# Optimization experiments

Measured on AMD Instinct MI355X. Metric: run time of the kernel, lower is better.

## Reference

```python
import jax, jax.numpy as jnp
import numpy as np


def setup_inputs() -> dict:
    key = jax.random.key(0)
    ks = jax.random.split(key, 8)
    B, E, L, D = 128, 512, 128, 128
    N = B * E
    return {
        "claim_vec": jax.random.normal(ks[0], (N, D), dtype=jnp.float32),
        "evidence_vec": jax.random.normal(ks[1], (N, D), dtype=jnp.float32),
        "ids_claim": jax.random.randint(ks[2], (N, L), 0, 30000, dtype=jnp.int64 if jax.config.jax_enable_x64 else jnp.int32),
        "ids_evidence": jax.random.randint(ks[3], (N, L), 0, 30000, dtype=jnp.int64 if jax.config.jax_enable_x64 else jnp.int32),
        "masks_claim": jax.random.randint(ks[4], (N, L), 0, 2, dtype=jnp.int64 if jax.config.jax_enable_x64 else jnp.int32),
        "masks_evidence": jax.random.randint(ks[5], (N, L), 0, 2, dtype=jnp.int64 if jax.config.jax_enable_x64 else jnp.int32),
        "token_claim": jax.random.randint(ks[6], (N, L), 0, 2, dtype=jnp.int64 if jax.config.jax_enable_x64 else jnp.int32),
        "token_evidence": jax.random.randint(ks[7], (N, L), 0, 2, dtype=jnp.int64 if jax.config.jax_enable_x64 else jnp.int32),
        "batchsize": 128,
        "evidences_num": 512,
        "top_k": 5,
        "max_len": 128,
    }


def reference(claim_vec, evidence_vec, ids_claim, ids_evidence,
              masks_claim, masks_evidence, token_claim, token_evidence,
              batchsize, evidences_num, top_k, max_len):
    B, E, K, L = batchsize, evidences_num, top_k, max_len
    eps = 1e-8
    # Cosine similarity per row (torch.F.cosine_similarity semantics: clamp each norm to eps)
    num = jnp.sum(claim_vec * evidence_vec, axis=-1)                      # [B*E]
    na = jnp.maximum(jnp.linalg.norm(claim_vec, axis=-1), eps)
    nb = jnp.maximum(jnp.linalg.norm(evidence_vec, axis=-1), eps)
    cos = (num / (na * nb)).reshape(B, E)
    cos_sim = jax.nn.softmax(cos, axis=1)
    top_cos, top_idx = jax.lax.top_k(cos_sim, K)                          # [B,K]

    def gather_ev(x):  # x: [B*E, L] -> top-k gathered, flattened [B*K, L]
        x3 = x.reshape(B, E, L)
        return jnp.take_along_axis(x3, top_idx[:, :, None], axis=1).reshape(-1, L)

    def slice_cl(x):   # claim side: first K rows per batch
        return x.reshape(B, E, L)[:, :K, :].reshape(-1, L)

    ids_retri = (slice_cl(ids_claim), gather_ev(ids_evidence))
    masks_retri = (slice_cl(masks_claim), gather_ev(masks_evidence))
    token_retri = (slice_cl(token_claim), gather_ev(token_evidence))
    return (top_cos, ids_retri[0], ids_retri[1], masks_retri[0], masks_retri[1],
            token_retri[0], token_retri[1])
```

## Files before the change

kernel.cpp:

```cpp
#include <hip/hip_runtime.h>
#include <hip/hip_bf16.h>
#include <math.h>

#define B_ 128
#define E_ 512
#define L_ 128
#define D_ 128
#define K_ 5
#define N_ (B_ * E_)
#define ROWOUT (B_ * K_)
#define OUT_TENSOR_SZ (ROWOUT * L_)

__global__ __launch_bounds__(256) void cos_kernel(const float* __restrict__ a,
                                                  const float* __restrict__ b,
                                                  float* __restrict__ cosout) {
    const int row  = blockIdx.x * 8 + (threadIdx.x >> 5);
    const int l32  = threadIdx.x & 31;
    const float4* a4 = reinterpret_cast<const float4*>(a) + (size_t)row * (D_ / 4) + l32;
    const float4* b4 = reinterpret_cast<const float4*>(b) + (size_t)row * (D_ / 4) + l32;
    float4 av = *a4;
    float4 bv = *b4;
    float dot = av.x * bv.x + av.y * bv.y + av.z * bv.z + av.w * bv.w;
    float na  = av.x * av.x + av.y * av.y + av.z * av.z + av.w * av.w;
    float nb  = bv.x * bv.x + bv.y * bv.y + bv.z * bv.z + bv.w * bv.w;
    #pragma unroll
    for (int o = 16; o; o >>= 1) {
        dot += __shfl_xor(dot, o);
        na  += __shfl_xor(na,  o);
        nb  += __shfl_xor(nb,  o);
    }
    if (l32 == 0) {
        const float eps = 1e-8f;
        float denom = fmaxf(sqrtf(na), eps) * fmaxf(sqrtf(nb), eps);
        cosout[row] = dot / denom;
    }
}

__global__ __launch_bounds__(512) void softmax_topk_gather_kernel(
        const float* __restrict__ cosv,
        const int* __restrict__ ids_c, const int* __restrict__ ids_e,
        const int* __restrict__ m_c,   const int* __restrict__ m_e,
        const int* __restrict__ t_c,   const int* __restrict__ t_e,
        float* __restrict__ out) {
    const int b    = blockIdx.x;
    const int e    = threadIdx.x;
    const int wid  = e >> 6;
    const int lane = e & 63;

    __shared__ float red[8];
    __shared__ float ps[E_];
    __shared__ int   topidx[K_];

    float v = cosv[b * E_ + e];

    float m = v;
    #pragma unroll
    for (int o = 32; o; o >>= 1) m = fmaxf(m, __shfl_xor(m, o));
    if (lane == 0) red[wid] = m;
    __syncthreads();
    float mall = red[0];
    #pragma unroll
    for (int i = 1; i < 8; i++) mall = fmaxf(mall, red[i]);
    __syncthreads();

    float ex = expf(v - mall);
    float s = ex;
    #pragma unroll
    for (int o = 32; o; o >>= 1) s += __shfl_xor(s, o);
    if (lane == 0) red[wid] = s;
    __syncthreads();
    float sall = 0.f;
    #pragma unroll
    for (int i = 0; i < 8; i++) sall += red[i];

    ps[e] = ex / sall;
    __syncthreads();

    if (wid == 0) {
        float vals[8];
        #pragma unroll
        for (int j = 0; j < 8; j++) vals[j] = ps[j * 64 + lane];

        for (int k = 0; k < K_; k++) {
            float val = vals[0];
            int   idx = lane;
            #pragma unroll
            for (int j = 1; j < 8; j++) {
                if (vals[j] > val) { val = vals[j]; idx = j * 64 + lane; }
            }
            #pragma unroll
            for (int o = 32; o; o >>= 1) {
                float ov = __shfl_xor(val, o);
                int   oi = __shfl_xor(idx, o);
                if (ov > val || (ov == val && oi < idx)) { val = ov; idx = oi; }
            }
            if (lane == 0) {
                out[b * K_ + k] = val;
                topidx[k] = idx;
            }
            #pragma unroll
            for (int j = 0; j < 8; j++) {
                if ((idx >> 6) == j && (idx & 63) == lane) vals[j] = -INFINITY;
            }
        }
    }
    __syncthreads();

    if (wid < K_) {
        const int k = wid;
        const int r = b * K_ + k;
        const size_t crow = (size_t)(b * E_ + k) * L_;
        const size_t erow = (size_t)(b * E_ + topidx[k]) * L_;
        const int q  = lane & 31;
        const int hi = lane >> 5;
        const int4* s0 = reinterpret_cast<const int4*>(hi ? (ids_e + erow) : (ids_c + crow));
        const int4* s1 = reinterpret_cast<const int4*>(hi ? (m_e   + erow) : (m_c   + crow));
        const int4* s2 = reinterpret_cast<const int4*>(hi ? (t_e   + erow) : (t_c   + crow));
        float4* d0 = reinterpret_cast<float4*>(out + 640 + (size_t)(0 + hi) * OUT_TENSOR_SZ + (size_t)r * L_);
        float4* d1 = reinterpret_cast<float4*>(out + 640 + (size_t)(2 + hi) * OUT_TENSOR_SZ + (size_t)r * L_);
        float4* d2 = reinterpret_cast<float4*>(out + 640 + (size_t)(4 + hi) * OUT_TENSOR_SZ + (size_t)r * L_);
        int4 v0 = s0[q];
        int4 v1 = s1[q];
        int4 v2 = s2[q];
        d0[q] = make_float4((float)v0.x, (float)v0.y, (float)v0.z, (float)v0.w);
        d1[q] = make_float4((float)v1.x, (float)v1.y, (float)v1.z, (float)v1.w);
        d2[q] = make_float4((float)v2.x, (float)v2.y, (float)v2.z, (float)v2.w);
    }
}

extern "C" void kernel_launch(void* const* d_in, const int* in_sizes, int n_in,
                              void* d_out, int out_size, void* d_ws, size_t ws_size,
                              hipStream_t stream) {
    const float* claim_vec    = (const float*)d_in[0];
    const float* evidence_vec = (const float*)d_in[1];
    const int*   ids_claim    = (const int*)d_in[2];
    const int*   ids_evidence = (const int*)d_in[3];
    const int*   masks_claim  = (const int*)d_in[4];
    const int*   masks_evid   = (const int*)d_in[5];
    const int*   token_claim  = (const int*)d_in[6];
    const int*   token_evid   = (const int*)d_in[7];

    float* cos_ws = (float*)d_ws;
    float* out    = (float*)d_out;

    cos_kernel<<<N_ / 8, 256, 0, stream>>>(claim_vec, evidence_vec, cos_ws);
    softmax_topk_gather_kernel<<<B_, 512, 0, stream>>>(cos_ws,
                                                       ids_claim, ids_evidence,
                                                       masks_claim, masks_evid,
                                                       token_claim, token_evid,
                                                       out);
}
```

Measured before the change: 22.77 us.

## Fuse cosine similarity into softmax/top-k/gather kernel, one block per batch

Merges the per-row cosine kernel into the softmax/top-k/gather kernel, so each of 128 blocks of 1024 threads computes its 512 cosines into shared memory, with a software-prefetched loop over 16 row groups. This removes the intermediate workspace round trip and one kernel launch. The cost is that the 64 MB vector read now runs on only 128 blocks, which may be too few to saturate HBM bandwidth on a 256-CU device.

```diff
diff --git a/kernel.cpp b/kernel.cpp
--- a/kernel.cpp
+++ b/kernel.cpp
@@ -1,5 +1,4 @@
 #include <hip/hip_runtime.h>
-#include <hip/hip_bf16.h>
 #include <math.h>
 
 #define B_ 128
@@ -11,69 +10,83 @@
 #define ROWOUT (B_ * K_)
 #define OUT_TENSOR_SZ (ROWOUT * L_)
 
-__global__ __launch_bounds__(256) void cos_kernel(const float* __restrict__ a,
-                                                  const float* __restrict__ b,
-                                                  float* __restrict__ cosout) {
-    const int row  = blockIdx.x * 8 + (threadIdx.x >> 5);
-    const int l32  = threadIdx.x & 31;
-    const float4* a4 = reinterpret_cast<const float4*>(a) + (size_t)row * (D_ / 4) + l32;
-    const float4* b4 = reinterpret_cast<const float4*>(b) + (size_t)row * (D_ / 4) + l32;
-    float4 av = *a4;
-    float4 bv = *b4;
-    float dot = av.x * bv.x + av.y * bv.y + av.z * bv.z + av.w * bv.w;
-    float na  = av.x * av.x + av.y * av.y + av.z * av.z + av.w * av.w;
-    float nb  = bv.x * bv.x + bv.y * bv.y + bv.z * bv.z + bv.w * bv.w;
-    #pragma unroll
-    for (int o = 16; o; o >>= 1) {
-        dot += __shfl_xor(dot, o);
-        na  += __shfl_xor(na,  o);
-        nb  += __shfl_xor(nb,  o);
-    }
-    if (l32 == 0) {
-        const float eps = 1e-8f;
-        float denom = fmaxf(sqrtf(na), eps) * fmaxf(sqrtf(nb), eps);
-        cosout[row] = dot / denom;
-    }
-}
-
-__global__ __launch_bounds__(512) void softmax_topk_gather_kernel(
-        const float* __restrict__ cosv,
+__global__ __launch_bounds__(1024) void fused_retriever_kernel(
+        const float* __restrict__ a,   const float* __restrict__ bvec,
         const int* __restrict__ ids_c, const int* __restrict__ ids_e,
         const int* __restrict__ m_c,   const int* __restrict__ m_e,
         const int* __restrict__ t_c,   const int* __restrict__ t_e,
         float* __restrict__ out) {
     const int b    = blockIdx.x;
-    const int e    = threadIdx.x;
-    const int wid  = e >> 6;
-    const int lane = e & 63;
+    const int t    = threadIdx.x;
+    const int h    = t >> 5;
+    const int l32  = t & 31;
+    const int lane = t & 63;
+    const int wid  = t >> 6;
 
+    __shared__ float cosv[E_];
+    __shared__ float ps[E_];
     __shared__ float red[8];
-    __shared__ float ps[E_];
     __shared__ int   topidx[K_];
 
-    float v = cosv[b * E_ + e];
+    const size_t rowbase = (size_t)b * E_;
+    const float4* ap = reinterpret_cast<const float4*>(a)    + (rowbase + h) * (D_ / 4) + l32;
+    const float4* bp = reinterpret_cast<const float4*>(bvec) + (rowbase + h) * (D_ / 4) + l32;
+    const int rstride = 32 * (D_ / 4);
 
-    float m = v;
+    float4 A0 = ap[0];
+    float4 B0 = bp[0];
     #pragma unroll
-    for (int o = 32; o; o >>= 1) m = fmaxf(m, __shfl_xor(m, o));
-    if (lane == 0) red[wid] = m;
-    __syncthreads();
-    float mall = red[0];
-    #pragma unroll
-    for (int i = 1; i < 8; i++) mall = fmaxf(mall, red[i]);
+    for (int it = 0; it < 16; ++it) {
+        float4 A1, B1;
+        if (it < 15) { A1 = ap[(it + 1) * rstride]; B1 = bp[(it + 1) * rstride]; }
+        float dot = A0.x * B0.x + A0.y * B0.y + A0.z * B0.z + A0.w * B0.w;
+        float na  = A0.x * A0.x + A0.y * A0.y + A0.z * A0.z + A0.w * A0.w;
+        float nb  = B0.x * B0.x + B0.y * B0.y + B0.z * B0.z + B0.w * B0.w;
+        #pragma unroll
+        for (int o = 16; o; o >>= 1) {
+            dot += __shfl_xor(dot, o);
+            na  += __shfl_xor(na,  o);
+            nb  += __shfl_xor(nb,  o);
+        }
+        if (l32 == 0) {
+            const float eps = 1e-8f;
+            float denom = fmaxf(sqrtf(na), eps) * fmaxf(sqrtf(nb), eps);
+            cosv[it * 32 + h] = dot / denom;
+        }
+        A0 = A1; B0 = B1;
+    }
     __syncthreads();
 
-    float ex = expf(v - mall);
-    float s = ex;
-    #pragma unroll
-    for (int o = 32; o; o >>= 1) s += __shfl_xor(s, o);
-    if (lane == 0) red[wid] = s;
+    float v = 0.f, ex = 0.f;
+    if (t < 512) {
+        v = cosv[t];
+        float m = v;
+        #pragma unroll
+        for (int o = 32; o; o >>= 1) m = fmaxf(m, __shfl_xor(m, o));
+        if (lane == 0) red[wid] = m;
+    }
     __syncthreads();
-    float sall = 0.f;
-    #pragma unroll
-    for (int i = 0; i < 8; i++) sall += red[i];
-
-    ps[e] = ex / sall;
+    float mall = 0.f;
+    if (t < 512) {
+        mall = red[0];
+        #pragma unroll
+        for (int i = 1; i < 8; i++) mall = fmaxf(mall, red[i]);
+    }
+    __syncthreads();
+    if (t < 512) {
+        ex = expf(v - mall);
+        float s = ex;
+        #pragma unroll
+        for (int o = 32; o; o >>= 1) s += __shfl_xor(s, o);
+        if (lane == 0) red[wid] = s;
+    }
+    __syncthreads();
+    if (t < 512) {
+        float sall = 0.f;
+        #pragma unroll
+        for (int i = 0; i < 8; i++) sall += red[i];
+        ps[t] = ex / sall;
+    }
     __syncthreads();
 
     if (wid == 0) {
@@ -119,12 +132,12 @@
         float4* d0 = reinterpret_cast<float4*>(out + 640 + (size_t)(0 + hi) * OUT_TENSOR_SZ + (size_t)r * L_);
         float4* d1 = reinterpret_cast<float4*>(out + 640 + (size_t)(2 + hi) * OUT_TENSOR_SZ + (size_t)r * L_);
         float4* d2 = reinterpret_cast<float4*>(out + 640 + (size_t)(4 + hi) * OUT_TENSOR_SZ + (size_t)r * L_);
-        int4 v0 = s0[q];
-        int4 v1 = s1[q];
-        int4 v2 = s2[q];
-        d0[q] = make_float4((float)v0.x, (float)v0.y, (float)v0.z, (float)v0.w);
-        d1[q] = make_float4((float)v1.x, (float)v1.y, (float)v1.z, (float)v1.w);
-        d2[q] = make_float4((float)v2.x, (float)v2.y, (float)v2.z, (float)v2.w);
+        int4 w0 = s0[q];
+        int4 w1 = s1[q];
+        int4 w2 = s2[q];
+        d0[q] = make_float4((float)w0.x, (float)w0.y, (float)w0.z, (float)w0.w);
+        d1[q] = make_float4((float)w1.x, (float)w1.y, (float)w1.z, (float)w1.w);
+        d2[q] = make_float4((float)w2.x, (float)w2.y, (float)w2.z, (float)w2.w);
     }
 }
 
@@ -140,13 +153,11 @@
     const int*   token_claim  = (const int*)d_in[6];
     const int*   token_evid   = (const int*)d_in[7];
 
-    float* cos_ws = (float*)d_ws;
-    float* out    = (float*)d_out;
+    float* out = (float*)d_out;
 
-    cos_kernel<<<N_ / 8, 256, 0, stream>>>(claim_vec, evidence_vec, cos_ws);
-    softmax_topk_gather_kernel<<<B_, 512, 0, stream>>>(cos_ws,
-                                                       ids_claim, ids_evidence,
-                                                       masks_claim, masks_evid,
-                                                       token_claim, token_evid,
-                                                       out);
+    fused_retriever_kernel<<<B_, 1024, 0, stream>>>(claim_vec, evidence_vec,
+                                                    ids_claim, ids_evidence,
+                                                    masks_claim, masks_evid,
+                                                    token_claim, token_evid,
+                                                    out);
 }
```

Result: slower. 23.97 us (+5.3%).
